# Kernel optimization log

Hardware: AMD Instinct MI355X
Metric: run time of the kernel (lower is better)

Reference implementation:

```python
import jax, jax.numpy as jnp
import numpy as np

N_NODES = 100000
N_EDGES = 3200000
IN_FEATS, N_HIDDEN, OUT_FEATS = 256, 128, 40


def setup_inputs() -> dict:
    key = jax.random.key(0)
    ks = jax.random.split(key, 8)
    x = jax.random.normal(ks[0], (N_NODES, IN_FEATS), dtype=jnp.float32)
    W0 = jax.random.normal(ks[1], (IN_FEATS, N_HIDDEN), dtype=jnp.float32) * (1.0 / np.sqrt(IN_FEATS))
    b0 = jnp.zeros((N_HIDDEN,), dtype=jnp.float32)
    W1 = jax.random.normal(ks[2], (N_HIDDEN, OUT_FEATS), dtype=jnp.float32) * (1.0 / np.sqrt(N_HIDDEN))
    b1 = jnp.zeros((OUT_FEATS,), dtype=jnp.float32)
    edge_weight = jax.random.uniform(ks[3], (N_EDGES,), dtype=jnp.float32)
    src = jax.random.randint(ks[4], (N_EDGES,), 0, N_NODES)
    dst = jax.random.randint(ks[5], (N_EDGES,), 0, N_NODES)
    return {"x": x, "W0": W0, "b0": b0, "W1": W1, "b1": b1,
            "edge_weight": edge_weight, "src": src, "dst": dst}


def reference(x, W0, b0, W1, b1, edge_weight, src, dst):
    n_nodes = x.shape[0]

    def gcn_conv(h, W, b):
        # linear transform first (PyG-style GCNConv), then sparse aggregate (SpMM)
        h = h @ W                                  # [N, d_out]
        msg = h[src] * edge_weight[:, None]        # [E, d_out] gathered + scaled
        agg = jax.ops.segment_sum(msg, dst, num_segments=n_nodes)  # scatter-add
        return agg + b

    h = jax.nn.relu(gcn_conv(x, W0, b0))
    out = gcn_conv(h, W1, b1)
    return jax.nn.log_softmax(out, axis=1)
```

## Files before the change

### kernel.cpp

```cpp
#include <hip/hip_runtime.h>
#include <hip/hip_bf16.h>
#include <cstdint>
#include <cstddef>

#define N_NODES   100000
#define N_EDGES   3200000
#define IN_FEATS  256
#define N_HIDDEN  128
#define OUT_FEATS 40

#define NB        196
#define EPB       8192
#define NBLK      391
#define HIST_M    (NB * NBLK)
#define N_TILES   3125
#define TPB       2
#define G0BLKS    ((N_TILES + TPB - 1) / TPB)

#if defined(__has_builtin)
#  if __has_builtin(__builtin_amdgcn_cvt_pk_f32_fp8) && \
      __has_builtin(__builtin_amdgcn_cvt_pk_fp8_f32)
#    define USE_FP8_H0 1
#  endif
#endif
#ifndef USE_FP8_H0
#  define USE_FP8_H0 0
#endif

typedef __attribute__((ext_vector_type(8))) __bf16 bf16x8;
typedef __attribute__((ext_vector_type(4))) float f32x4;
typedef __attribute__((ext_vector_type(2))) float f32x2;

__device__ __forceinline__ void pkfma(f32x2& a, unsigned int u, f32x2 w2) {
  f32x2 b;
  b.x = __uint_as_float(u << 16);
  b.y = __uint_as_float(u & 0xFFFF0000u);
  a += b * w2;
}

#define ACC8P(A_, V_, W2_)   \
  pkfma(A_[0], (V_).x, W2_); \
  pkfma(A_[1], (V_).y, W2_); \
  pkfma(A_[2], (V_).z, W2_); \
  pkfma(A_[3], (V_).w, W2_);

#if USE_FP8_H0
#define FP8ACC(A_, V_, W2_) {                                          \
  f32x2 d_;                                                            \
  d_ = __builtin_amdgcn_cvt_pk_f32_fp8((V_).x, false); A_[0] += d_ * (W2_); \
  d_ = __builtin_amdgcn_cvt_pk_f32_fp8((V_).x, true ); A_[1] += d_ * (W2_); \
  d_ = __builtin_amdgcn_cvt_pk_f32_fp8((V_).y, false); A_[2] += d_ * (W2_); \
  d_ = __builtin_amdgcn_cvt_pk_f32_fp8((V_).y, true ); A_[3] += d_ * (W2_); \
  d_ = __builtin_amdgcn_cvt_pk_f32_fp8((V_).z, false); A_[4] += d_ * (W2_); \
  d_ = __builtin_amdgcn_cvt_pk_f32_fp8((V_).z, true ); A_[5] += d_ * (W2_); \
  d_ = __builtin_amdgcn_cvt_pk_f32_fp8((V_).w, false); A_[6] += d_ * (W2_); \
  d_ = __builtin_amdgcn_cvt_pk_f32_fp8((V_).w, true ); A_[7] += d_ * (W2_); }
#endif

__device__ __forceinline__ void gemm0_block(
    int bid, const float* __restrict__ x, const uint4* __restrict__ w0f,
    unsigned char* __restrict__ h0) {
  __shared__ __align__(16) unsigned short xb[32 * 264];
  const int tid  = threadIdx.x;
  const int lane = tid & 63;
  const int wave = tid >> 6;
  const int rb   = wave & 1;
  const int ch   = wave >> 1;
  const int l15  = lane & 15;
  const int g    = lane >> 4;

  bf16x8 Bf[4][8];
#pragma unroll
  for (int cb = 0; cb < 4; ++cb)
#pragma unroll
    for (int q = 0; q < 8; ++q)
      Bf[cb][q] = __builtin_bit_cast(bf16x8, w0f[((ch * 4 + cb) * 8 + q) * 64 + lane]);

  for (int t = 0; t < TPB; ++t) {
    const int tile = bid * TPB + t;
    if (tile >= N_TILES) break;
    const int row0 = tile * 32;
    __syncthreads();
    for (int i = tid; i < 32 * 128; i += 256) {
      const int row = i >> 7, kp = i & 127;
      const float2 v = *(const float2*)(x + (size_t)(row0 + row) * IN_FEATS + kp * 2);
      __hip_bfloat162 p;
      p.x = __float2bfloat16(v.x);
      p.y = __float2bfloat16(v.y);
      *(unsigned int*)&xb[row * 264 + kp * 2] = *(unsigned int*)&p;
    }
    __syncthreads();

    f32x4 acc[4];
#pragma unroll
    for (int cb = 0; cb < 4; ++cb) acc[cb] = (f32x4){0.f, 0.f, 0.f, 0.f};

#pragma unroll
    for (int q = 0; q < 8; ++q) {
      const bf16x8 a = *(const bf16x8*)&xb[(rb * 16 + l15) * 264 + q * 32 + g * 8];
      acc[0] = __builtin_amdgcn_mfma_f32_16x16x32_bf16(a, Bf[0][q], acc[0], 0, 0, 0);
      acc[1] = __builtin_amdgcn_mfma_f32_16x16x32_bf16(a, Bf[1][q], acc[1], 0, 0, 0);
      acc[2] = __builtin_amdgcn_mfma_f32_16x16x32_bf16(a, Bf[2][q], acc[2], 0, 0, 0);
      acc[3] = __builtin_amdgcn_mfma_f32_16x16x32_bf16(a, Bf[3][q], acc[3], 0, 0, 0);
    }

#pragma unroll
    for (int cb = 0; cb < 4; ++cb) {
      const int col = ch * 64 + cb * 16 + l15;
#pragma unroll
      for (int r = 0; r < 4; ++r) {
        const int row = row0 + rb * 16 + g * 4 + r;
#if USE_FP8_H0
        const int pk = __builtin_amdgcn_cvt_pk_fp8_f32(acc[cb][r], acc[cb][r], 0, false);
        h0[(size_t)row * N_HIDDEN + col] = (unsigned char)(pk & 0xFF);
#else
        __hip_bfloat16 hb = __float2bfloat16(acc[cb][r]);
        ((unsigned short*)h0)[(size_t)row * N_HIDDEN + col] = *(unsigned short*)&hb;
#endif
      }
    }
  }
}

__device__ __forceinline__ void bucket_scan_block(
    int b, const int* __restrict__ bsum, int* __restrict__ histG) {
  __shared__ int sh[256];
  __shared__ int pr[256];
  const int t = threadIdx.x;

  sh[t] = (t < b) ? bsum[t] : 0;
  __syncthreads();
#pragma unroll
  for (int off = 128; off > 0; off >>= 1) {
    if (t < off) sh[t] += sh[t + off];
    __syncthreads();
  }
  const int base = sh[0];

  const int row = b * NBLK;
  const int i0 = 2 * t, i1 = 2 * t + 1;
  int a = 0, c = 0;
  if (t < 196) {
    a = histG[row + i0];
    if (i1 < NBLK) c = histG[row + i1];
  }
  pr[t] = a + c;
  __syncthreads();
  for (int off = 1; off < 256; off <<= 1) {
    int v = (t >= off) ? pr[t - off] : 0;
    __syncthreads();
    pr[t] += v;
    __syncthreads();
  }
  if (t < 196) {
    const int ebase = (t > 0) ? pr[t - 1] : 0;
    histG[row + i0] = base + ebase;
    if (i1 < NBLK) histG[row + i1] = base + ebase + a;
  }
}

__global__ __launch_bounds__(256) void bscan_kernel(
    const int* __restrict__ bsum, int* __restrict__ histG) {
  bucket_scan_block(blockIdx.x, bsum, histG);
}

__global__ __launch_bounds__(256) void p1hist_kernel(
    const int* __restrict__ dst, int* __restrict__ histG,
    const float* __restrict__ W1, uint4* __restrict__ w1f,
    const float* __restrict__ W0, uint4* __restrict__ w0f,
    int* __restrict__ bsum) {
  const int tid = threadIdx.x;
  const int blk = blockIdx.x;

  if (blk >= NBLK) {
    if (blk == NBLK) {
      for (int t = tid; t < 3 * 4 * 64; t += 256) {
        const int ln  = t & 63;
        const int qq  = (t >> 6) & 3;
        const int nt  = t >> 8;
        const int l15 = ln & 15;
        const int gg  = ln >> 4;
        const int c   = nt * 16 + l15;
        const int k0  = qq * 32 + gg * 8;
        uint4 u;
        __hip_bfloat162 p;
#define W1AT(i_) ((c < OUT_FEATS) ? W1[(size_t)(k0 + (i_)) * OUT_FEATS + c] : 0.f)
        p.x = __float2bfloat16(W1AT(0)); p.y = __float2bfloat16(W1AT(1));
        u.x = *(unsigned int*)&p;
        p.x = __float2bfloat16(W1AT(2)); p.y = __float2bfloat16(W1AT(3));
        u.y = *(unsigned int*)&p;
        p.x = __float2bfloat16(W1AT(4)); p.y = __float2bfloat16(W1AT(5));
        u.z = *(unsigned int*)&p;
        p.x = __float2bfloat16(W1AT(6)); p.y = __float2bfloat16(W1AT(7));
        u.w = *(unsigned int*)&p;
#undef W1AT
        w1f[t] = u;
      }
    } else {
      const int pb = blk - NBLK - 1;
      for (int fi = pb * 512 + tid; fi < pb * 512 + 512; fi += 256) {
        const int ln  = fi & 63;
        const int qq  = (fi >> 6) & 7;
        const int ct  = fi >> 9;
        const int col = ct * 16 + (ln & 15);
        const int k0  = qq * 32 + (ln >> 4) * 8;
        uint4 u;
        __hip_bfloat162 p;
        p.x = __float2bfloat16(W0[(size_t)(k0 + 0) * N_HIDDEN + col]);
        p.y = __float2bfloat16(W0[(size_t)(k0 + 1) * N_HIDDEN + col]);
        u.x = *(unsigned int*)&p;
        p.x = __float2bfloat16(W0[(size_t)(k0 + 2) * N_HIDDEN + col]);
        p.y = __float2bfloat16(W0[(size_t)(k0 + 3) * N_HIDDEN + col]);
        u.y = *(unsigned int*)&p;
        p.x = __float2bfloat16(W0[(size_t)(k0 + 4) * N_HIDDEN + col]);
        p.y = __float2bfloat16(W0[(size_t)(k0 + 5) * N_HIDDEN + col]);
        u.z = *(unsigned int*)&p;
        p.x = __float2bfloat16(W0[(size_t)(k0 + 6) * N_HIDDEN + col]);
        p.y = __float2bfloat16(W0[(size_t)(k0 + 7) * N_HIDDEN + col]);
        u.w = *(unsigned int*)&p;
        w0f[fi] = u;
      }
    }
    return;
  }

  __shared__ int lh[NB];
  for (int i = tid; i < NB; i += 256) lh[i] = 0;
  __syncthreads();

  const int e0 = blk * EPB;
  const int e1 = min(e0 + EPB, N_EDGES);
  for (int i = e0 + tid; i < e1; i += 256)
    atomicAdd(&lh[dst[i] >> 9], 1);
  __syncthreads();

  for (int i = tid; i < NB; i += 256) {
    histG[i * NBLK + blk] = lh[i];
    atomicAdd(&bsum[i], lh[i]);
  }
}

__global__ __launch_bounds__(256) void p1scatter_kernel(
    const int* __restrict__ src, const int* __restrict__ dst,
    const float* __restrict__ ew, const int* __restrict__ histG,
    uint2* __restrict__ bucketed) {
  __shared__ uint2 stage[EPB];
  __shared__ unsigned char sbkt[EPB];
  __shared__ int lcnt[NB];
  __shared__ int lbase[NB];
  __shared__ int spart[256];
  const int tid = threadIdx.x;
  const int blk = blockIdx.x;
  const int e0 = blk * EPB;
  const int e1 = min(e0 + EPB, N_EDGES);

  for (int i = tid; i < NB; i += 256) lcnt[i] = 0;
  __syncthreads();

  for (int i = e0 + tid; i < e1; i += 256)
    atomicAdd(&lcnt[dst[i] >> 9], 1);
  __syncthreads();

  const int myv = (tid < NB) ? lcnt[tid] : 0;
  spart[tid] = myv;
  __syncthreads();
  for (int off = 1; off < 256; off <<= 1) {
    int u = (tid >= off) ? spart[tid - off] : 0;
    __syncthreads();
    spart[tid] += u;
    __syncthreads();
  }
  if (tid < NB) { lbase[tid] = spart[tid] - myv; lcnt[tid] = spart[tid] - myv; }
  __syncthreads();

  for (int i = e0 + tid; i < e1; i += 256) {
    const int d = dst[i];
    const int b = d >> 9;
    const int pos = atomicAdd(&lcnt[b], 1);
    stage[pos] = make_uint2((unsigned)src[i] | ((unsigned)(d & 511) << 17),
                            __float_as_uint(ew[i]));
    sbkt[pos] = (unsigned char)b;
  }
  __syncthreads();

  const int n = e1 - e0;
  for (int i = tid; i < n; i += 256) {
    const int b = sbkt[i];
    const int gpos = histG[b * NBLK + blk] + (i - lbase[b]);
    bucketed[gpos] = stage[i];
  }
}

__device__ __forceinline__ void p2place_block(
    int b, const uint2* __restrict__ bucketed, const int* __restrict__ histG,
    int* __restrict__ offsets, int2* __restrict__ srcw) {
  __shared__ int cnt[512];
  __shared__ int part[256];
  const int t = threadIdx.x;
  const int node0 = b << 9;
  const int beg = histG[b * NBLK];
  const int end = (b == NB - 1) ? N_EDGES : histG[(b + 1) * NBLK];

  cnt[t] = 0; cnt[t + 256] = 0;
  __syncthreads();

  for (int j = beg + t; j < end; j += 256)
    atomicAdd(&cnt[bucketed[j].x >> 17], 1);
  __syncthreads();

  const int a0 = cnt[2 * t];
  const int a1 = cnt[2 * t + 1];
  part[t] = a0 + a1;
  __syncthreads();
  for (int off = 1; off < 256; off <<= 1) {
    int v = (t >= off) ? part[t - off] : 0;
    __syncthreads();
    part[t] += v;
    __syncthreads();
  }
  const int base = (t > 0) ? part[t - 1] : 0;

  const int o0 = beg + base;
  const int o1 = o0 + a0;
  cnt[2 * t]     = o0;
  cnt[2 * t + 1] = o1;
  const int n0 = node0 + 2 * t;
  if (n0 < N_NODES)     offsets[n0]     = o0;
  if (n0 + 1 < N_NODES) offsets[n0 + 1] = o1;
  if (b == NB - 1 && t == 0) offsets[N_NODES] = N_EDGES;
  __syncthreads();

  for (int j = beg + t; j < end; j += 256) {
    const uint2 en = bucketed[j];
    const int slot = atomicAdd(&cnt[en.x >> 17], 1);
    srcw[slot] = make_int2((int)(en.x & 0x1FFFFu), (int)en.y);
  }
}

__global__ __launch_bounds__(256) void place_gemm0_kernel(
    const uint2* __restrict__ bucketed, const int* __restrict__ histG,
    int* __restrict__ offsets, int2* __restrict__ srcw,
    const float* __restrict__ x, const uint4* __restrict__ w0f,
    unsigned char* __restrict__ h0) {
  if (blockIdx.x < NB) p2place_block(blockIdx.x, bucketed, histG, offsets, srcw);
  else                 gemm0_block(blockIdx.x - NB, x, w0f, h0);
}

#if USE_FP8_H0
__global__ __launch_bounds__(256) void gather0_gemm1_kernel(
    const uint4* __restrict__ h0q, const int2* __restrict__ srcw,
    const int* __restrict__ offsets, const float* __restrict__ b0,
    const uint4* __restrict__ w1f, unsigned short* __restrict__ h1a,
    unsigned short* __restrict__ h1c) {
  __shared__ float hs[4][132];
  const int wave = threadIdx.x >> 6;
  const int lane = threadIdx.x & 63;
  const int node = blockIdx.x * 4 + wave;
  const int g  = lane >> 3;
  const int fl = lane & 7;

  const int beg = __builtin_amdgcn_readfirstlane(offsets[node]);
  const int end = __builtin_amdgcn_readfirstlane(offsets[node + 1]);

  f32x2 acc[8];
#pragma unroll
  for (int i = 0; i < 8; ++i) acc[i] = (f32x2){0.f, 0.f};

  if (end > beg) {
    const int e1 = end - 1;
    int2 sa = srcw[min(beg + g, e1)];
    int2 sb = srcw[min(beg + 8 + g, e1)];
    for (int j = beg; j < end; j += 16) {
      const float wa = (j + g < end)     ? __int_as_float(sa.y) : 0.f;
      const float wb = (j + 8 + g < end) ? __int_as_float(sb.y) : 0.f;
      const uint4 va = h0q[(size_t)(unsigned)sa.x * 8 + fl];
      const uint4 vb = h0q[(size_t)(unsigned)sb.x * 8 + fl];
      const int jn = j + 16;
      if (jn < end) {
        sa = srcw[min(jn + g, e1)];
        sb = srcw[min(jn + 8 + g, e1)];
      }
      const f32x2 pa = {wa, wa};
      const f32x2 pb = {wb, wb};
      FP8ACC(acc, va, pa)
      FP8ACC(acc, vb, pb)
    }
  }

#pragma unroll
  for (int i = 0; i < 8; ++i) {
    acc[i].x += __shfl_xor(acc[i].x, 8);
    acc[i].x += __shfl_xor(acc[i].x, 16);
    acc[i].x += __shfl_xor(acc[i].x, 32);
    acc[i].y += __shfl_xor(acc[i].y, 8);
    acc[i].y += __shfl_xor(acc[i].y, 16);
    acc[i].y += __shfl_xor(acc[i].y, 32);
  }

  if (g == 0) {
    const int f0 = fl * 16;
#pragma unroll
    for (int jj = 0; jj < 4; ++jj) {
      const float v0 = acc[2 * jj].x     + b0[f0 + 4 * jj + 0];
      const float v1 = acc[2 * jj].y     + b0[f0 + 4 * jj + 1];
      const float v2 = acc[2 * jj + 1].x + b0[f0 + 4 * jj + 2];
      const float v3 = acc[2 * jj + 1].y + b0[f0 + 4 * jj + 3];
      *(float4*)&hs[wave][f0 + 4 * jj] = make_float4(
          v0 > 0.f ? v0 : 0.f, v1 > 0.f ? v1 : 0.f,
          v2 > 0.f ? v2 : 0.f, v3 > 0.f ? v3 : 0.f);
    }
  }
  __syncthreads();

  const int l15 = lane & 15;
  const int gg  = lane >> 4;
  if (wave < 3) {
    f32x4 c = {0.f, 0.f, 0.f, 0.f};
#pragma unroll
    for (int qq = 0; qq < 4; ++qq) {
      uint4 ua = make_uint4(0, 0, 0, 0);
      if (l15 < 4) {
        const float* hrow = &hs[l15][qq * 32 + gg * 8];
        __hip_bfloat162 p;
        p.x = __float2bfloat16(hrow[0]); p.y = __float2bfloat16(hrow[1]);
        ua.x = *(unsigned int*)&p;
        p.x = __float2bfloat16(hrow[2]); p.y = __float2bfloat16(hrow[3]);
        ua.y = *(unsigned int*)&p;
        p.x = __float2bfloat16(hrow[4]); p.y = __float2bfloat16(hrow[5]);
        ua.z = *(unsigned int*)&p;
        p.x = __float2bfloat16(hrow[6]); p.y = __float2bfloat16(hrow[7]);
        ua.w = *(unsigned int*)&p;
      }
      const uint4 ub = w1f[(wave * 4 + qq) * 64 + lane];
      c = __builtin_amdgcn_mfma_f32_16x16x32_bf16(
            __builtin_bit_cast(bf16x8, ua), __builtin_bit_cast(bf16x8, ub),
            c, 0, 0, 0);
    }
    if (gg == 0) {
#pragma unroll
      for (int r = 0; r < 4; ++r) {
        const int nodeR = blockIdx.x * 4 + r;
        const int f = wave * 16 + l15;
        __hip_bfloat16 hb = __float2bfloat16(c[r]);
        const unsigned short v16 = *(unsigned short*)&hb;
        if (f < 32)              h1a[(size_t)nodeR * 32 + f] = v16;
        else if (f < OUT_FEATS)  h1c[(size_t)nodeR * 8 + (f - 32)] = v16;
      }
    }
  }
}
#else
__global__ __launch_bounds__(256) void gather0_gemm1_kernel(
    const uint4* __restrict__ h0q, const int2* __restrict__ srcw,
    const int* __restrict__ offsets, const float* __restrict__ b0,
    const uint4* __restrict__ w1f, unsigned short* __restrict__ h1a,
    unsigned short* __restrict__ h1c) {
  __shared__ float hs[4][132];
  const int wave = threadIdx.x >> 6;
  const int lane = threadIdx.x & 63;
  const int node = blockIdx.x * 4 + wave;
  const int q    = lane >> 4;
  const int fl   = lane & 15;

  const int beg = __builtin_amdgcn_readfirstlane(offsets[node]);
  const int end = __builtin_amdgcn_readfirstlane(offsets[node + 1]);

  f32x2 acc[4];
#pragma unroll
  for (int i = 0; i < 4; ++i) acc[i] = (f32x2){0.f, 0.f};

  if (end > beg) {
    const int e1 = end - 1;
    int2 sa = srcw[min(beg + q, e1)];
    int2 sb = srcw[min(beg + 4 + q, e1)];
    int2 sc = srcw[min(beg + 8 + q, e1)];
    int2 sd = srcw[min(beg + 12 + q, e1)];
    for (int j = beg; j < end; j += 16) {
      const float wa = (j + q < end)      ? __int_as_float(sa.y) : 0.f;
      const float wb = (j + 4 + q < end)  ? __int_as_float(sb.y) : 0.f;
      const float wc = (j + 8 + q < end)  ? __int_as_float(sc.y) : 0.f;
      const float wd = (j + 12 + q < end) ? __int_as_float(sd.y) : 0.f;
      const uint4 va = h0q[(size_t)(unsigned)sa.x * 16 + fl];
      const uint4 vb = h0q[(size_t)(unsigned)sb.x * 16 + fl];
      const uint4 vc = h0q[(size_t)(unsigned)sc.x * 16 + fl];
      const uint4 vd = h0q[(size_t)(unsigned)sd.x * 16 + fl];
      const int jn = j + 16;
      if (jn < end) {
        sa = srcw[min(jn + q, e1)];
        sb = srcw[min(jn + 4 + q, e1)];
        sc = srcw[min(jn + 8 + q, e1)];
        sd = srcw[min(jn + 12 + q, e1)];
      }
      const f32x2 pa = {wa, wa};
      const f32x2 pb = {wb, wb};
      const f32x2 pc = {wc, wc};
      const f32x2 pd = {wd, wd};
      ACC8P(acc, va, pa)
      ACC8P(acc, vb, pb)
      ACC8P(acc, vc, pc)
      ACC8P(acc, vd, pd)
    }
  }

#pragma unroll
  for (int i = 0; i < 4; ++i) {
    acc[i].x += __shfl_xor(acc[i].x, 16);
    acc[i].x += __shfl_xor(acc[i].x, 32);
    acc[i].y += __shfl_xor(acc[i].y, 16);
    acc[i].y += __shfl_xor(acc[i].y, 32);
  }

  if (q == 0) {
    const int f0 = fl * 8;
    float t[8];
#pragma unroll
    for (int i = 0; i < 8; ++i) {
      const float a = ((i & 1) ? acc[i >> 1].y : acc[i >> 1].x);
      const float v = a + b0[f0 + i];
      t[i] = v > 0.f ? v : 0.f;
    }
    *(float4*)&hs[wave][f0]     = make_float4(t[0], t[1], t[2], t[3]);
    *(float4*)&hs[wave][f0 + 4] = make_float4(t[4], t[5], t[6], t[7]);
  }
  __syncthreads();

  const int l15 = lane & 15;
  const int gg  = lane >> 4;
  if (wave < 3) {
    f32x4 c = {0.f, 0.f, 0.f, 0.f};
#pragma unroll
    for (int qq = 0; qq < 4; ++qq) {
      uint4 ua = make_uint4(0, 0, 0, 0);
      if (l15 < 4) {
        const float* hrow = &hs[l15][qq * 32 + gg * 8];
        __hip_bfloat162 p;
        p.x = __float2bfloat16(hrow[0]); p.y = __float2bfloat16(hrow[1]);
        ua.x = *(unsigned int*)&p;
        p.x = __float2bfloat16(hrow[2]); p.y = __float2bfloat16(hrow[3]);
        ua.y = *(unsigned int*)&p;
        p.x = __float2bfloat16(hrow[4]); p.y = __float2bfloat16(hrow[5]);
        ua.z = *(unsigned int*)&p;
        p.x = __float2bfloat16(hrow[6]); p.y = __float2bfloat16(hrow[7]);
        ua.w = *(unsigned int*)&p;
      }
      const uint4 ub = w1f[(wave * 4 + qq) * 64 + lane];
      c = __builtin_amdgcn_mfma_f32_16x16x32_bf16(
            __builtin_bit_cast(bf16x8, ua), __builtin_bit_cast(bf16x8, ub),
            c, 0, 0, 0);
    }
    if (gg == 0) {
#pragma unroll
      for (int r = 0; r < 4; ++r) {
        const int nodeR = blockIdx.x * 4 + r;
        const int f = wave * 16 + l15;
        __hip_bfloat16 hb = __float2bfloat16(c[r]);
        const unsigned short v16 = *(unsigned short*)&hb;
        if (f < 32)              h1a[(size_t)nodeR * 32 + f] = v16;
        else if (f < OUT_FEATS)  h1c[(size_t)nodeR * 8 + (f - 32)] = v16;
      }
    }
  }
}
#endif

__global__ __launch_bounds__(256) void gather1_lsm_kernel(
    const uint4* __restrict__ h1aq, const unsigned int* __restrict__ h1cd,
    const int2* __restrict__ srcw, const int* __restrict__ offsets,
    const float* __restrict__ b1, float* __restrict__ out) {
  const int wave = threadIdx.x >> 6;
  const int lane = threadIdx.x & 63;
  const int node = blockIdx.x * 4 + wave;
  const int g  = lane >> 2;
  const int fl = lane & 3;

  const int beg = __builtin_amdgcn_readfirstlane(offsets[node]);
  const int end = __builtin_amdgcn_readfirstlane(offsets[node + 1]);

  f32x2 acc[4];
  f32x2 accc = {0.f, 0.f};
#pragma unroll
  for (int i = 0; i < 4; ++i) acc[i] = (f32x2){0.f, 0.f};

  if (end > beg) {
    const int e1 = end - 1;
    int2 sa = srcw[min(beg + g, e1)];
    int2 sb = srcw[min(beg + 16 + g, e1)];
    for (int j = beg; j < end; j += 32) {
      const float wa = (j + g < end)      ? __int_as_float(sa.y) : 0.f;
      const float wb = (j + 16 + g < end) ? __int_as_float(sb.y) : 0.f;
      const uint4 va = h1aq[(size_t)(unsigned)sa.x * 4 + fl];
      const uint4 vb = h1aq[(size_t)(unsigned)sb.x * 4 + fl];
      const unsigned int ca = h1cd[(size_t)(unsigned)sa.x * 4 + fl];
      const unsigned int cb = h1cd[(size_t)(unsigned)sb.x * 4 + fl];
      const int jn = j + 32;
      if (jn < end) {
        sa = srcw[min(jn + g, e1)];
        sb = srcw[min(jn + 16 + g, e1)];
      }
      const f32x2 pa = {wa, wa};
      const f32x2 pb = {wb, wb};
      ACC8P(acc, va, pa)
      pkfma(accc, ca, pa);
      ACC8P(acc, vb, pb)
      pkfma(accc, cb, pb);
    }
  }

  float o[8], oc0, oc1;
#pragma unroll
  for (int i = 0; i < 4; ++i) {
    float x0 = acc[i].x, y0 = acc[i].y;
    x0 += __shfl_xor(x0, 4); x0 += __shfl_xor(x0, 8);
    x0 += __shfl_xor(x0, 16); x0 += __shfl_xor(x0, 32);
    y0 += __shfl_xor(y0, 4); y0 += __shfl_xor(y0, 8);
    y0 += __shfl_xor(y0, 16); y0 += __shfl_xor(y0, 32);
    o[2 * i] = x0; o[2 * i + 1] = y0;
  }
  {
    float x0 = accc.x, y0 = accc.y;
    x0 += __shfl_xor(x0, 4); x0 += __shfl_xor(x0, 8);
    x0 += __shfl_xor(x0, 16); x0 += __shfl_xor(x0, 32);
    y0 += __shfl_xor(y0, 4); y0 += __shfl_xor(y0, 8);
    y0 += __shfl_xor(y0, 16); y0 += __shfl_xor(y0, 32);
    oc0 = x0; oc1 = y0;
  }

  const int f0 = fl * 8;
  float m = -INFINITY;
#pragma unroll
  for (int i = 0; i < 8; ++i) {
    o[i] += b1[f0 + i];
    m = fmaxf(m, o[i]);
  }
  oc0 += b1[32 + 2 * fl];
  oc1 += b1[33 + 2 * fl];
  m = fmaxf(m, oc0);
  m = fmaxf(m, oc1);
  m = fmaxf(m, __shfl_xor(m, 1));
  m = fmaxf(m, __shfl_xor(m, 2));

  float s = 0.f;
#pragma unroll
  for (int i = 0; i < 8; ++i) s += expf(o[i] - m);
  s += expf(oc0 - m) + expf(oc1 - m);
  s += __shfl_xor(s, 1);
  s += __shfl_xor(s, 2);

  if (lane < 4) {
    const float lse = m + logf(s);
    float* op = out + (size_t)node * OUT_FEATS;
    *(float4*)(op + f0)     = make_float4(o[0] - lse, o[1] - lse,
                                          o[2] - lse, o[3] - lse);
    *(float4*)(op + f0 + 4) = make_float4(o[4] - lse, o[5] - lse,
                                          o[6] - lse, o[7] - lse);
    *(float2*)(op + 32 + 2 * fl) = make_float2(oc0 - lse, oc1 - lse);
  }
}

extern "C" void kernel_launch(void* const* d_in, const int* in_sizes, int n_in,
                              void* d_out, int out_size, void* d_ws, size_t ws_size,
                              hipStream_t stream) {
  const float* x   = (const float*)d_in[0];
  const float* W0  = (const float*)d_in[1];
  const float* b0  = (const float*)d_in[2];
  const float* W1  = (const float*)d_in[3];
  const float* b1  = (const float*)d_in[4];
  const float* ew  = (const float*)d_in[5];
  const int*   src = (const int*)d_in[6];
  const int*   dst = (const int*)d_in[7];
  float* out = (float*)d_out;

  char* ws = (char*)d_ws;
  unsigned char* h0 = (unsigned char*)(ws);
  int2*  srcw     = (int2*)(ws + 25600000);
  uint2* bucketed = (uint2*)(ws + 51200000);
  int*   offsets  = (int*)(ws + 76800000);
  int*   histG    = (int*)(ws + 77200064);
  unsigned short* h1a = (unsigned short*)(ws + 77506624);
  unsigned short* h1c = (unsigned short*)(ws + 83906624);
  uint4* w1f      = (uint4*)(ws + 85506624);
  uint4* w0f      = (uint4*)(ws + 85518912);
  int*   bsum     = (int*)(ws + 85584448);

  hipMemsetAsync(bsum, 0, NB * sizeof(int), stream);
  p1hist_kernel<<<NBLK + 9, 256, 0, stream>>>(dst, histG, W1, w1f, W0, w0f, bsum);
  bscan_kernel<<<NB, 256, 0, stream>>>(bsum, histG);
  p1scatter_kernel<<<NBLK, 256, 0, stream>>>(src, dst, ew, histG, bucketed);
  place_gemm0_kernel<<<NB + G0BLKS, 256, 0, stream>>>(
      bucketed, histG, offsets, srcw, x, w0f, h0);
  gather0_gemm1_kernel<<<N_NODES / 4, 256, 0, stream>>>(
      (const uint4*)h0, srcw, offsets, b0, (const uint4*)w1f, h1a, h1c);
  gather1_lsm_kernel<<<N_NODES / 4, 256, 0, stream>>>(
      (const uint4*)h1a, (const unsigned int*)h1c, srcw, offsets, b1, out);
}
```

Measured before the change: 443.4 us.

## Stage CSR placement through LDS in two halves and widen fused blocks to 512

The placement phase now puts each bucket's edges into a large LDS staging buffer, one half of the 512 nodes at a time. Each staged half is then written to srcw contiguously instead of as scattered per-edge stores. Overflow past the staging capacity falls back to direct global writes. The fused kernel moves to 512 threads, so each gemm0 wave computes 32 output columns instead of 64 and holds fewer registers. The trade-offs are that the bucketed array is read three times instead of twice, and every block, including the gemm0 blocks, reserves about 76 KB of shared memory, which limits occupancy.

```diff
diff --git a/kernel.cpp b/kernel.cpp
--- a/kernel.cpp
+++ b/kernel.cpp
@@ -16,6 +16,7 @@
 #define N_TILES   3125
 #define TPB       2
 #define G0BLKS    ((N_TILES + TPB - 1) / TPB)
+#define STCAP     8960
 
 #if defined(__has_builtin)
 #  if __has_builtin(__builtin_amdgcn_cvt_pk_f32_fp8) && \
@@ -59,8 +60,8 @@
 
 __device__ __forceinline__ void gemm0_block(
     int bid, const float* __restrict__ x, const uint4* __restrict__ w0f,
-    unsigned char* __restrict__ h0) {
-  __shared__ __align__(16) unsigned short xb[32 * 264];
+    unsigned char* __restrict__ h0, char* smem) {
+  unsigned short* xb = (unsigned short*)smem;
   const int tid  = threadIdx.x;
   const int lane = tid & 63;
   const int wave = tid >> 6;
@@ -69,19 +70,19 @@
   const int l15  = lane & 15;
   const int g    = lane >> 4;
 
-  bf16x8 Bf[4][8];
-#pragma unroll
-  for (int cb = 0; cb < 4; ++cb)
+  bf16x8 Bf[2][8];
+#pragma unroll
+  for (int cb = 0; cb < 2; ++cb)
 #pragma unroll
     for (int q = 0; q < 8; ++q)
-      Bf[cb][q] = __builtin_bit_cast(bf16x8, w0f[((ch * 4 + cb) * 8 + q) * 64 + lane]);
+      Bf[cb][q] = __builtin_bit_cast(bf16x8, w0f[((ch * 2 + cb) * 8 + q) * 64 + lane]);
 
   for (int t = 0; t < TPB; ++t) {
     const int tile = bid * TPB + t;
     if (tile >= N_TILES) break;
     const int row0 = tile * 32;
     __syncthreads();
-    for (int i = tid; i < 32 * 128; i += 256) {
+    for (int i = tid; i < 32 * 128; i += 512) {
       const int row = i >> 7, kp = i & 127;
       const float2 v = *(const float2*)(x + (size_t)(row0 + row) * IN_FEATS + kp * 2);
       __hip_bfloat162 p;
@@ -91,22 +92,20 @@
     }
     __syncthreads();
 
-    f32x4 acc[4];
-#pragma unroll
-    for (int cb = 0; cb < 4; ++cb) acc[cb] = (f32x4){0.f, 0.f, 0.f, 0.f};
+    f32x4 acc[2];
+#pragma unroll
+    for (int cb = 0; cb < 2; ++cb) acc[cb] = (f32x4){0.f, 0.f, 0.f, 0.f};
 
 #pragma unroll
     for (int q = 0; q < 8; ++q) {
       const bf16x8 a = *(const bf16x8*)&xb[(rb * 16 + l15) * 264 + q * 32 + g * 8];
       acc[0] = __builtin_amdgcn_mfma_f32_16x16x32_bf16(a, Bf[0][q], acc[0], 0, 0, 0);
       acc[1] = __builtin_amdgcn_mfma_f32_16x16x32_bf16(a, Bf[1][q], acc[1], 0, 0, 0);
-      acc[2] = __builtin_amdgcn_mfma_f32_16x16x32_bf16(a, Bf[2][q], acc[2], 0, 0, 0);
-      acc[3] = __builtin_amdgcn_mfma_f32_16x16x32_bf16(a, Bf[3][q], acc[3], 0, 0, 0);
-    }
-
-#pragma unroll
-    for (int cb = 0; cb < 4; ++cb) {
-      const int col = ch * 64 + cb * 16 + l15;
+    }
+
+#pragma unroll
+    for (int cb = 0; cb < 2; ++cb) {
+      const int col = ch * 32 + cb * 16 + l15;
 #pragma unroll
       for (int r = 0; r < 4; ++r) {
         const int row = row0 + rb * 16 + g * 4 + r;
@@ -122,10 +121,99 @@
   }
 }
 
-__device__ __forceinline__ void bucket_scan_block(
-    int b, const int* __restrict__ bsum, int* __restrict__ histG) {
+__device__ __forceinline__ void p2place_block(
+    int b, const uint2* __restrict__ bucketed, const int* __restrict__ histG,
+    int* __restrict__ offsets, int2* __restrict__ srcw, char* smem) {
+  int*   cnt   = (int*)smem;
+  int*   part  = (int*)(smem + 2048);
+  int*   sb    = (int*)(smem + 4096);
+  uint2* stage = (uint2*)(smem + 4112);
+  const int t = threadIdx.x;
+  const int node0 = b << 9;
+  const int beg = histG[b * NBLK];
+  const int end = (b == NB - 1) ? N_EDGES : histG[(b + 1) * NBLK];
+
+  cnt[t] = 0;
+  __syncthreads();
+
+  for (int j = beg + t; j < end; j += 512)
+    atomicAdd(&cnt[bucketed[j].x >> 17], 1);
+  __syncthreads();
+
+  const int myv = cnt[t];
+  part[t] = myv;
+  __syncthreads();
+  for (int off = 1; off < 512; off <<= 1) {
+    int v = (t >= off) ? part[t - off] : 0;
+    __syncthreads();
+    part[t] += v;
+    __syncthreads();
+  }
+  const int excl = part[t] - myv;
+
+  const int nd = node0 + t;
+  if (nd < N_NODES) offsets[nd] = beg + excl;
+  if (b == NB - 1 && t == 0) offsets[N_NODES] = N_EDGES;
+  if (t == 255) sb[0] = part[255];
+  __syncthreads();
+  const int h0cnt = sb[0];
+  const int h1cnt = (end - beg) - h0cnt;
+
+  cnt[t] = excl;
+  __syncthreads();
+
+  for (int j = beg + t; j < end; j += 512) {
+    const uint2 e = bucketed[j];
+    const int ln = e.x >> 17;
+    if (ln < 256) {
+      const int pos = atomicAdd(&cnt[ln], 1);
+      if (pos < STCAP) stage[pos] = e;
+      else srcw[beg + pos] = make_int2((int)(e.x & 0x1FFFFu), (int)e.y);
+    }
+  }
+  __syncthreads();
+  const int w0 = min(h0cnt, STCAP);
+  for (int i = t; i < w0; i += 512) {
+    const uint2 e = stage[i];
+    srcw[beg + i] = make_int2((int)(e.x & 0x1FFFFu), (int)e.y);
+  }
+  __syncthreads();
+
+  for (int j = beg + t; j < end; j += 512) {
+    const uint2 e = bucketed[j];
+    const int ln = e.x >> 17;
+    if (ln >= 256) {
+      const int pos = atomicAdd(&cnt[ln], 1);
+      const int ph = pos - h0cnt;
+      if (ph < STCAP) stage[ph] = e;
+      else srcw[beg + pos] = make_int2((int)(e.x & 0x1FFFFu), (int)e.y);
+    }
+  }
+  __syncthreads();
+  const int w1 = min(h1cnt, STCAP);
+  for (int i = t; i < w1; i += 512) {
+    const uint2 e = stage[i];
+    srcw[beg + h0cnt + i] = make_int2((int)(e.x & 0x1FFFFu), (int)e.y);
+  }
+}
+
+__global__ __launch_bounds__(512) void place_gemm0_kernel(
+    const uint2* __restrict__ bucketed, const int* __restrict__ histG,
+    int* __restrict__ offsets, int2* __restrict__ srcw,
+    const float* __restrict__ x, const uint4* __restrict__ w0f,
+    unsigned char* __restrict__ h0) {
+  __shared__ __align__(16) char smem[4112 + STCAP * 8];
+  if (blockIdx.x < NB)
+    p2place_block(blockIdx.x, bucketed, histG, offsets, srcw, smem);
+  else
+    gemm0_block(blockIdx.x - NB, x, w0f, h0, smem);
+}
+
+__global__ __launch_bounds__(256) void bscan_kernel(
+    const int* __restrict__ bsum, int* __restrict__ histG) {
   __shared__ int sh[256];
   __shared__ int pr[256];
+  const int b = blockIdx.x;
   const int t = threadIdx.x;
 
   sh[t] = (t < b) ? bsum[t] : 0;
@@ -157,11 +245,6 @@
     histG[row + i0] = base + ebase;
     if (i1 < NBLK) histG[row + i1] = base + ebase + a;
   }
-}
-
-__global__ __launch_bounds__(256) void bscan_kernel(
-    const int* __restrict__ bsum, int* __restrict__ histG) {
-  bucket_scan_block(blockIdx.x, bsum, histG);
 }
 
 __global__ __launch_bounds__(256) void p1hist_kernel(
@@ -291,61 +374,6 @@
   }
 }
 
-__device__ __forceinline__ void p2place_block(
-    int b, const uint2* __restrict__ bucketed, const int* __restrict__ histG,
-    int* __restrict__ offsets, int2* __restrict__ srcw) {
-  __shared__ int cnt[512];
-  __shared__ int part[256];
-  const int t = threadIdx.x;
-  const int node0 = b << 9;
-  const int beg = histG[b * NBLK];
-  const int end = (b == NB - 1) ? N_EDGES : histG[(b + 1) * NBLK];
-
-  cnt[t] = 0; cnt[t + 256] = 0;
-  __syncthreads();
-
-  for (int j = beg + t; j < end; j += 256)
-    atomicAdd(&cnt[bucketed[j].x >> 17], 1);
-  __syncthreads();
-
-  const int a0 = cnt[2 * t];
-  const int a1 = cnt[2 * t + 1];
-  part[t] = a0 + a1;
-  __syncthreads();
-  for (int off = 1; off < 256; off <<= 1) {
-    int v = (t >= off) ? part[t - off] : 0;
-    __syncthreads();
-    part[t] += v;
-    __syncthreads();
-  }
-  const int base = (t > 0) ? part[t - 1] : 0;
-
-  const int o0 = beg + base;
-  const int o1 = o0 + a0;
-  cnt[2 * t]     = o0;
-  cnt[2 * t + 1] = o1;
-  const int n0 = node0 + 2 * t;
-  if (n0 < N_NODES)     offsets[n0]     = o0;
-  if (n0 + 1 < N_NODES) offsets[n0 + 1] = o1;
-  if (b == NB - 1 && t == 0) offsets[N_NODES] = N_EDGES;
-  __syncthreads();
-
-  for (int j = beg + t; j < end; j += 256) {
-    const uint2 en = bucketed[j];
-    const int slot = atomicAdd(&cnt[en.x >> 17], 1);
-    srcw[slot] = make_int2((int)(en.x & 0x1FFFFu), (int)en.y);
-  }
-}
-
-__global__ __launch_bounds__(256) void place_gemm0_kernel(
-    const uint2* __restrict__ bucketed, const int* __restrict__ histG,
-    int* __restrict__ offsets, int2* __restrict__ srcw,
-    const float* __restrict__ x, const uint4* __restrict__ w0f,
-    unsigned char* __restrict__ h0) {
-  if (blockIdx.x < NB) p2place_block(blockIdx.x, bucketed, histG, offsets, srcw);
-  else                 gemm0_block(blockIdx.x - NB, x, w0f, h0);
-}
-
 #if USE_FP8_H0
 __global__ __launch_bounds__(256) void gather0_gemm1_kernel(
     const uint4* __restrict__ h0q, const int2* __restrict__ srcw,
@@ -686,7 +714,7 @@
   p1hist_kernel<<<NBLK + 9, 256, 0, stream>>>(dst, histG, W1, w1f, W0, w0f, bsum);
   bscan_kernel<<<NB, 256, 0, stream>>>(bsum, histG);
   p1scatter_kernel<<<NBLK, 256, 0, stream>>>(src, dst, ew, histG, bucketed);
-  place_gemm0_kernel<<<NB + G0BLKS, 256, 0, stream>>>(
+  place_gemm0_kernel<<<NB + G0BLKS, 512, 0, stream>>>(
       bucketed, histG, offsets, srcw, x, w0f, h0);
   gather0_gemm1_kernel<<<N_NODES / 4, 256, 0, stream>>>(
       (const uint4*)h0, srcw, offsets, b0, (const uint4*)w1f, h1a, h1c);
```

Result: no change. 436.9 us (-1.5%).
